# Optimization experiments

Measured on AMD Instinct MI355X. Metric: run time of the kernel, lower is better.

## Reference

```python
import jax, jax.numpy as jnp
import numpy as np

N_ATOMS = 65536
N_PAIRS = N_ATOMS * 32
MAXZ = 95          # D3 tables cover H..Pu, indexed directly by atomic number
NREF = 5           # number of reference coordination numbers per element
CUTOFF, CUTON = 12.0, 10.0   # model units; distances_model2Bohr == 1
K1, K3 = 16.0, -4.0
SMALL = 1e-30      # fp32 stand-in for the original's 1e-300 double guard


def setup_inputs() -> dict:
    key = jax.random.key(0)
    k0, k1, k2, k3 = jax.random.split(key, 4)
    rng = np.random.default_rng(0)

    atomic_numbers = jax.random.randint(k0, (N_ATOMS,), 1, 87)
    idx_i = jax.random.randint(k1, (N_PAIRS,), 0, N_ATOMS)
    idx_j = jax.random.randint(k2, (N_PAIRS,), 0, N_ATOMS)
    # pair distances spanning inside/switch/outside of the 10..12 cutoff band
    distances = jax.random.uniform(k3, (N_PAIRS,), minval=0.8, maxval=12.5)

    # synthetic stand-ins for the grimme_d3 data files
    rcov = jnp.asarray(rng.uniform(0.5, 3.0, (MAXZ,)).astype(np.float32))
    rcn_np = rng.uniform(0.0, 5.0, (MAXZ, NREF)).astype(np.float32)
    rcn_np[::3, NREF - 1] = -1.0  # mimic -1 padding for missing references
    rcn = jnp.asarray(rcn_np)
    rc6 = jnp.asarray(rng.uniform(1.0, 50.0, (MAXZ, MAXZ, NREF, NREF)).astype(np.float32))
    r2r4 = jnp.asarray(rng.uniform(1.0, 10.0, (MAXZ,)).astype(np.float32))

    s6 = jnp.float32(1.0)
    s8 = jnp.float32(0.9171)
    a1 = jnp.float32(0.3385)
    a2 = jnp.float32(2.883)
    return dict(distances=distances, rcov=rcov, rcn=rcn, rc6=rc6, r2r4=r2r4,
                s6=s6, s8=s8, a1=a1, a2=a2,
                atomic_numbers=atomic_numbers, idx_i=idx_i, idx_j=idx_j)


def reference(distances, rcov, rcn, rc6, r2r4, s6, s8, a1, a2,
              atomic_numbers, idx_i, idx_j):
    n = atomic_numbers.shape[0]
    zi = atomic_numbers[idx_i]
    zj = atomic_numbers[idx_j]

    # smooth switch-off from 1 (r < cuton) to 0 (r >= cutoff)
    x = (CUTOFF - distances) / (CUTOFF - CUTON)
    sw = jnp.where(distances < CUTON, 1.0,
                   jnp.where(distances >= CUTOFF, 0.0,
                             ((6.0 * x - 15.0) * x + 10.0) * x * x * x))

    # coordination numbers via inverse damping, scatter-summed per atom i
    rcov_ij = rcov[zi] + rcov[zj]
    cn_ij = sw / (1.0 + jnp.exp(-K1 * (rcov_ij / distances - 1.0)))
    cn = jax.ops.segment_sum(cn_ij, idx_i, num_segments=n)  # [N]

    # Gaussian weights over reference CNs (soft retrieval into rc6 table)
    rcn_a = rcn[atomic_numbers]                 # [N, NREF]
    mask = rcn_a >= 0
    dcn = rcn_a - cn[:, None]
    gw = jnp.where(mask, jnp.exp(K3 * dcn * dcn), 0.0)
    norm = jnp.sum(gw, axis=-1, keepdims=True)
    # exceptional case: all gaussians underflow -> pick the max reference CN
    rcn_max_a = jnp.max(rcn, axis=-1)[atomic_numbers][:, None]
    exceptional = (rcn_a == rcn_max_a).astype(gw.dtype)
    weights = jnp.where(norm == 0, exceptional, gw / jnp.maximum(norm, SMALL))  # [N, NREF]

    # weighted pairwise C6 from reference table rc6[Zi, Zj, a, b]
    w_i = weights[idx_i]                         # [P, NREF]
    w_j = weights[idx_j]                         # [P, NREF]
    c6 = jnp.einsum('pa,pb,pab->p', w_i, w_j, rc6[zi, zj])

    # C8 = 3 * C6 * <r2>/<r4>_i * <r2>/<r4>_j ; BJ critical radius
    qq = 3.0 * r2r4[zi] * r2r4[zj]
    rr = a1 * jnp.sqrt(qq) + a2

    d2 = distances * distances
    d6 = d2 * d2 * d2
    d8 = d6 * d2
    rr2 = rr * rr
    rr6 = rr2 * rr2 * rr2
    rr8 = rr6 * rr2

    # BJ-damped dispersion energy per pair (0.5 for double counting), switched
    e_pair = -0.5 * (s6 * c6 / (d6 + rr6) + s8 * qq * c6 / (d8 + rr8)) * sw

    # per-atom dispersion energies (energies_Hartree2model == 1)
    return jax.ops.segment_sum(e_pair, idx_i, num_segments=n)
```

## Files before the change

kernel.cpp:

```cpp
#include <hip/hip_runtime.h>
#include <stdint.h>


typedef unsigned short u16;
#define MAXZ 95
#define NREF 5
#define EXC_CUT -87.33654f
#define NB    1024
#define BSH   6
#define BSZ   64
#define CAPSH 12
#define SBLOCKS 128
#define RC_TOTAL (MAXZ * MAXZ * 32)

__device__ __forceinline__ float h2f(u16 h) {
    union { _Float16 h; u16 u; } v; v.u = h; return (float)v.h;
}
__device__ __forceinline__ u16 f2h(float f) {
    union { _Float16 h; u16 u; } v; v.h = (_Float16)f; return v.u;
}

__device__ __forceinline__ float switch_fn(float d) {
    if (d < 10.0f) return 1.0f;
    float x = (12.0f - d) * 0.5f;
    return ((6.0f * x - 15.0f) * x + 10.0f) * x * x * x;
}

__device__ __forceinline__ void calc_weights(const float* __restrict__ rcn_z,
                                             float cni, float* __restrict__ w) {
    float r[NREF], arg[NREF];
    float rmax = -1e30f, marg = -1e30f;
#pragma unroll
    for (int a = 0; a < NREF; a++) {
        r[a] = rcn_z[a];
        rmax = fmaxf(rmax, r[a]);
        float dc = r[a] - cni;
        arg[a] = (-4.0f * dc) * dc;
        if (r[a] >= 0.0f) marg = fmaxf(marg, arg[a]);
    }
    if (marg < EXC_CUT) {
#pragma unroll
        for (int a = 0; a < NREF; a++) w[a] = (r[a] == rmax) ? 1.0f : 0.0f;
    } else {
        float g[NREF], norm = 0.0f;
#pragma unroll
        for (int a = 0; a < NREF; a++) {
            float e = (r[a] >= 0.0f) ? expf(arg[a]) : 0.0f;
            g[a] = e;
            norm += e;
        }
        float inv = 1.0f / fmaxf(norm, 1e-30f);
#pragma unroll
        for (int a = 0; a < NREF; a++) w[a] = g[a] * inv;
    }
}

__global__ __launch_bounds__(1024) void scatter_pairs(const float* __restrict__ dist,
                                                      const int* __restrict__ idx_i,
                                                      const int* __restrict__ idx_j,
                                                      const int* __restrict__ Z,
                                                      const float* __restrict__ rcov,
                                                      const float* __restrict__ rc6,
                                                      float* __restrict__ rcovA,
                                                      u16* __restrict__ rc6pad,
                                                      uint32_t* __restrict__ bcount,
                                                      uint2* __restrict__ recs,
                                                      int n_pairs, int n_atoms,
                                                      int chunk) {
    __shared__ uint32_t hist[NB];
    __shared__ uint32_t run[NB];

    int g = blockIdx.x * 1024 + (int)threadIdx.x;
    int T = gridDim.x * 1024;
    for (int i = g; i < n_atoms; i += T) rcovA[i] = rcov[Z[i]];
    for (int id = g; id < RC_TOTAL; id += T) {
        int tile = id >> 5, slot = id & 31;
        rc6pad[id] = (slot < 25) ? f2h(rc6[(size_t)tile * 25 + slot]) : (u16)0;
    }

    for (int t = threadIdx.x; t < NB; t += 1024) hist[t] = 0;
    __syncthreads();
    int lo = blockIdx.x * chunk;
    int hi = min(lo + chunk, n_pairs);

    for (int q0 = lo + (int)threadIdx.x * 4; q0 < hi; q0 += 4096) {
        int m = min(4, hi - q0);
        float d4[4];
        int i4[4];
        if (m == 4) {
            float4 dv = *(const float4*)(dist + q0);
            int4 iv = *(const int4*)(idx_i + q0);
            d4[0] = dv.x; d4[1] = dv.y; d4[2] = dv.z; d4[3] = dv.w;
            i4[0] = iv.x; i4[1] = iv.y; i4[2] = iv.z; i4[3] = iv.w;
        } else {
            for (int s = 0; s < m; s++) { d4[s] = dist[q0 + s]; i4[s] = idx_i[q0 + s]; }
        }
#pragma unroll
        for (int s = 0; s < 4; s++) {
            if (s < m && d4[s] < 12.0f)
                atomicAdd(&hist[((uint32_t)i4[s]) >> BSH], 1u);
        }
    }
    __syncthreads();
    for (int t = threadIdx.x; t < NB; t += 1024) {
        uint32_t h = hist[t];
        run[t] = h ? atomicAdd(&bcount[t], h) : 0u;
    }
    __syncthreads();

    for (int q0 = lo + (int)threadIdx.x * 4; q0 < hi; q0 += 4096) {
        int m = min(4, hi - q0);
        float d4[4];
        int i4[4], j4[4];
        if (m == 4) {
            float4 dv = *(const float4*)(dist + q0);
            int4 iv = *(const int4*)(idx_i + q0);
            int4 jv = *(const int4*)(idx_j + q0);
            d4[0] = dv.x; d4[1] = dv.y; d4[2] = dv.z; d4[3] = dv.w;
            i4[0] = iv.x; i4[1] = iv.y; i4[2] = iv.z; i4[3] = iv.w;
            j4[0] = jv.x; j4[1] = jv.y; j4[2] = jv.z; j4[3] = jv.w;
        } else {
            for (int s = 0; s < m; s++) {
                d4[s] = dist[q0 + s]; i4[s] = idx_i[q0 + s]; j4[s] = idx_j[q0 + s];
            }
        }
#pragma unroll
        for (int s = 0; s < 4; s++) {
            if (s >= m) continue;
            float d = d4[s];
            if (d >= 12.0f) continue;
            uint32_t i = (uint32_t)i4[s];
            uint32_t b = i >> BSH;
            uint32_t pos = atomicAdd(&run[b], 1u);
            if (pos < (1u << CAPSH)) {
                uint32_t packed = ((uint32_t)j4[s] & 0xFFFFu) |
                                  ((i & (BSZ - 1u)) << 16);
                recs[((size_t)b << CAPSH) + pos] = make_uint2(__float_as_uint(d), packed);
            }
        }
    }
}

__global__ __launch_bounds__(256) void cn_weights_bucket(const uint2* __restrict__ recs,
                                                         const uint32_t* __restrict__ bcount,
                                                         const float* __restrict__ rcovA,
                                                         const int* __restrict__ Z,
                                                         const float* __restrict__ rcn,
                                                         const float* __restrict__ r2r4,
                                                         uint4* __restrict__ arec_h,
                                                         int n_atoms) {
    __shared__ float lrc[BSZ];
    __shared__ float acc[BSZ];
    int b = blockIdx.x;
    int base = b << BSH;
    if (threadIdx.x < BSZ) {
        int i = base + (int)threadIdx.x;
        lrc[threadIdx.x] = (i < n_atoms) ? rcovA[i] : 0.0f;
        acc[threadIdx.x] = 0.0f;
    }
    __syncthreads();
    uint32_t n = min(bcount[b], 1u << CAPSH);
    const uint2* r0 = recs + ((size_t)b << CAPSH);
    for (uint32_t k = threadIdx.x; k < n; k += 256) {
        uint2 r = r0[k];
        float d = __uint_as_float(r.x);
        int j  = r.y & 0xFFFF;
        int il = r.y >> 16;
        float rij = lrc[il] + rcovA[j];
        float sw = switch_fn(d);
        atomicAdd(&acc[il], sw / (1.0f + expf(-16.0f * (rij / d - 1.0f))));
    }
    __syncthreads();
    if (threadIdx.x < BSZ) {
        int i = base + (int)threadIdx.x;
        if (i < n_atoms) {
            int z = Z[i];
            float w[NREF];
            calc_weights(rcn + (size_t)z * NREF, acc[threadIdx.x], w);
            uint4 pk;
            pk.x = (uint32_t)f2h(w[0]) | ((uint32_t)f2h(w[1]) << 16);
            pk.y = (uint32_t)f2h(w[2]) | ((uint32_t)f2h(w[3]) << 16);
            pk.z = (uint32_t)f2h(w[4]) | ((uint32_t)f2h(r2r4[z]) << 16);
            pk.w = (uint32_t)z;
            arec_h[i] = pk;
        }
    }
}

__global__ __launch_bounds__(256) void energy_bucket(const uint2* __restrict__ recs,
                                                     const uint32_t* __restrict__ bcount,
                                                     const uint4* __restrict__ arec_h,
                                                     const u16* __restrict__ rc6pad,
                                                     const float* __restrict__ s6p,
                                                     const float* __restrict__ s8p,
                                                     const float* __restrict__ a1p,
                                                     const float* __restrict__ a2p,
                                                     float* __restrict__ eout,
                                                     int n_atoms) {
    __shared__ float4 la0[BSZ];
    __shared__ float4 la1[BSZ];
    __shared__ float  acc[BSZ];
    int b = blockIdx.x;
    int base = b << BSH;
    if (threadIdx.x < BSZ) {
        int i = min(base + (int)threadIdx.x, n_atoms - 1);
        uint4 pk = arec_h[i];
        la0[threadIdx.x] = make_float4(h2f(pk.x & 0xFFFFu), h2f(pk.x >> 16),
                                       h2f(pk.y & 0xFFFFu), h2f(pk.y >> 16));
        la1[threadIdx.x] = make_float4(h2f(pk.z & 0xFFFFu), h2f(pk.z >> 16),
                                       __int_as_float((int)pk.w), 0.0f);
        acc[threadIdx.x] = 0.0f;
    }
    __syncthreads();
    float s6 = s6p[0], s8 = s8p[0], a1 = a1p[0], a2 = a2p[0];
    uint32_t n = min(bcount[b], 1u << CAPSH);
    const uint2* r0 = recs + ((size_t)b << CAPSH);
    for (uint32_t k = threadIdx.x; k < n; k += 256) {
        uint2 r = r0[k];
        float d = __uint_as_float(r.x);
        int j  = r.y & 0xFFFF;
        int il = r.y >> 16;
        float4 ai0 = la0[il];
        float4 ai1 = la1[il];
        uint4 pj = arec_h[j];
        float wj[NREF] = {h2f(pj.x & 0xFFFFu), h2f(pj.x >> 16),
                          h2f(pj.y & 0xFFFFu), h2f(pj.y >> 16),
                          h2f(pj.z & 0xFFFFu)};
        float r2r4j = h2f(pj.z >> 16);
        int zi = __float_as_int(ai1.z);
        int zj = (int)pj.w;
        float wi[NREF] = {ai0.x, ai0.y, ai0.z, ai0.w, ai1.x};

        const uint4* T4 = (const uint4*)(rc6pad + (size_t)(zi * MAXZ + zj) * 32);
        uint4 t0 = T4[0], t1 = T4[1], t2 = T4[2];
        uint32_t t3 = ((const uint32_t*)T4)[12];
        float tt[25];
        uint32_t tw[12] = {t0.x, t0.y, t0.z, t0.w, t1.x, t1.y, t1.z, t1.w,
                           t2.x, t2.y, t2.z, t2.w};
#pragma unroll
        for (int k2 = 0; k2 < 12; k2++) {
            tt[2 * k2]     = h2f((u16)(tw[k2] & 0xFFFFu));
            tt[2 * k2 + 1] = h2f((u16)(tw[k2] >> 16));
        }
        tt[24] = h2f((u16)(t3 & 0xFFFFu));

        float c6 = 0.0f;
#pragma unroll
        for (int a = 0; a < NREF; a++) {
            float ss = 0.0f;
#pragma unroll
            for (int bb = 0; bb < NREF; bb++) ss = fmaf(wj[bb], tt[a * NREF + bb], ss);
            c6 = fmaf(wi[a], ss, c6);
        }

        float qq = 3.0f * ai1.y * r2r4j;
        float rr = a1 * sqrtf(qq) + a2;
        float d2 = d * d;
        float d6 = d2 * d2 * d2;
        float d8 = d6 * d2;
        float rr2 = rr * rr;
        float rr6 = rr2 * rr2 * rr2;
        float rr8 = rr6 * rr2;
        float sw = switch_fn(d);

        float e = -0.5f * (s6 * c6 / (d6 + rr6) + s8 * qq * c6 / (d8 + rr8)) * sw;
        atomicAdd(&acc[il], e);
    }
    __syncthreads();
    if (threadIdx.x < BSZ) {
        int i = base + (int)threadIdx.x;
        if (i < n_atoms) eout[i] = acc[threadIdx.x];
    }
}

__global__ __launch_bounds__(256) void pair_cn_slim(const float* __restrict__ dist,
                                                    const float* __restrict__ rcov,
                                                    const int* __restrict__ Z,
                                                    const int* __restrict__ idx_i,
                                                    const int* __restrict__ idx_j,
                                                    float* __restrict__ cn,
                                                    int n_pairs) {
    int p = blockIdx.x * blockDim.x + threadIdx.x;
    if (p >= n_pairs) return;
    float d = dist[p];
    if (d >= 12.0f) return;
    float rij = rcov[Z[idx_i[p]]] + rcov[Z[idx_j[p]]];
    float sw = switch_fn(d);
    atomicAdd(&cn[idx_i[p]], sw / (1.0f + expf(-16.0f * (rij / d - 1.0f))));
}

__global__ __launch_bounds__(256) void pair_energy_slim(const float* __restrict__ dist,
                                                        const int* __restrict__ Z,
                                                        const int* __restrict__ idx_i,
                                                        const int* __restrict__ idx_j,
                                                        const float* __restrict__ cn,
                                                        const float* __restrict__ rcn,
                                                        const float* __restrict__ r2r4,
                                                        const float* __restrict__ rc6,
                                                        const float* __restrict__ s6p,
                                                        const float* __restrict__ s8p,
                                                        const float* __restrict__ a1p,
                                                        const float* __restrict__ a2p,
                                                        float* __restrict__ eout,
                                                        int n_pairs) {
    int p = blockIdx.x * blockDim.x + threadIdx.x;
    if (p >= n_pairs) return;
    float d = dist[p];
    if (d >= 12.0f) return;
    int i = idx_i[p], j = idx_j[p];
    int zi = Z[i], zj = Z[j];
    float wi[NREF], wj[NREF];
    calc_weights(rcn + (size_t)zi * NREF, cn[i], wi);
    calc_weights(rcn + (size_t)zj * NREF, cn[j], wj);
    const float* T = rc6 + (size_t)(zi * MAXZ + zj) * 25;
    float c6 = 0.0f;
#pragma unroll
    for (int a = 0; a < NREF; a++) {
        float s = 0.0f;
#pragma unroll
        for (int bb = 0; bb < NREF; bb++) s = fmaf(wj[bb], T[a * NREF + bb], s);
        c6 = fmaf(wi[a], s, c6);
    }
    float qq = 3.0f * r2r4[zi] * r2r4[zj];
    float rr = a1p[0] * sqrtf(qq) + a2p[0];
    float d2 = d * d;
    float d6 = d2 * d2 * d2;
    float d8 = d6 * d2;
    float rr2 = rr * rr;
    float rr6 = rr2 * rr2 * rr2;
    float rr8 = rr6 * rr2;
    float sw = switch_fn(d);
    float e = -0.5f * (s6p[0] * c6 / (d6 + rr6) + s8p[0] * qq * c6 / (d8 + rr8)) * sw;
    atomicAdd(&eout[i], e);
}

extern "C" void kernel_launch(void* const* d_in, const int* in_sizes, int n_in,
                              void* d_out, int out_size, void* d_ws, size_t ws_size,
                              hipStream_t stream) {
    const float* dist = (const float*)d_in[0];
    const float* rcov = (const float*)d_in[1];
    const float* rcn  = (const float*)d_in[2];
    const float* rc6  = (const float*)d_in[3];
    const float* r2r4 = (const float*)d_in[4];
    const float* s6p  = (const float*)d_in[5];
    const float* s8p  = (const float*)d_in[6];
    const float* a1p  = (const float*)d_in[7];
    const float* a2p  = (const float*)d_in[8];
    const int* Z    = (const int*)d_in[9];
    const int* idxi = (const int*)d_in[10];
    const int* idxj = (const int*)d_in[11];
    float* out = (float*)d_out;

    int n_pairs = in_sizes[0];
    int n_atoms = in_sizes[9];

    char* ws = (char*)d_ws;
    size_t o_bcount = 0;
    size_t o_rcovA  = 4096;
    size_t o_arec   = (o_rcovA + (size_t)n_atoms * 4 + 15) & ~(size_t)15;
    size_t o_rc6    = (o_arec + (size_t)n_atoms * 16 + 63) & ~(size_t)63;
    size_t o_recs   = (o_rc6 + (size_t)RC_TOTAL * 2 + 255) & ~(size_t)255;
    size_t need     = o_recs + ((size_t)NB << CAPSH) * 8;

    uint32_t* bcount = (uint32_t*)(ws + o_bcount);
    float* rcovA  = (float*)(ws + o_rcovA);
    uint4* arec_h = (uint4*)(ws + o_arec);
    u16*   rcpad  = (u16*)(ws + o_rc6);
    uint2* recs   = (uint2*)(ws + o_recs);

    if (ws_size >= need && n_atoms <= NB * BSZ && n_atoms <= 65536) {
        hipMemsetAsync(bcount, 0, NB * 4, stream);
        int chunk = (n_pairs + SBLOCKS - 1) / SBLOCKS;
        scatter_pairs<<<SBLOCKS, 1024, 0, stream>>>(dist, idxi, idxj, Z, rcov, rc6,
                                                    rcovA, rcpad, bcount, recs,
                                                    n_pairs, n_atoms, chunk);
        cn_weights_bucket<<<NB, 256, 0, stream>>>(recs, bcount, rcovA, Z, rcn, r2r4,
                                                  arec_h, n_atoms);
        energy_bucket<<<NB, 256, 0, stream>>>(recs, bcount, arec_h, rcpad,
                                              s6p, s8p, a1p, a2p, out, n_atoms);
    } else {
        int pgrid = (n_pairs + 255) / 256;
        float* cn = (float*)(ws + o_rcovA);
        hipMemsetAsync(out, 0, (size_t)n_atoms * 4, stream);
        hipMemsetAsync(cn, 0, (size_t)n_atoms * 4, stream);
        pair_cn_slim<<<pgrid, 256, 0, stream>>>(dist, rcov, Z, idxi, idxj, cn, n_pairs);
        pair_energy_slim<<<pgrid, 256, 0, stream>>>(dist, Z, idxi, idxj, cn, rcn, r2r4,
                                                    rc6, s6p, s8p, a1p, a2p, out, n_pairs);
    }
}
```

Before: 147.2 us.

## Pack neighbor atomic number into pair records to remove gathers

The scatter kernel now gathers Z[j] once per in-cutoff pair and packs it into the upper bits of the record word. The CN kernel then looks up rcov from a shared-memory table indexed by that Z instead of gathering a per-atom rcovA array, which is no longer built. The energy kernel takes zj from the record so the rc6 tile load can be issued before the arec_h[j] gather, and the loads are reordered to overlap. This adds a random Z gather in the scatter pass and relies on j fitting in 16 bits and Z in 7 bits.

```diff
diff --git a/kernel.cpp b/kernel.cpp
--- a/kernel.cpp
+++ b/kernel.cpp
@@ -59,20 +59,16 @@
                                                       const int* __restrict__ idx_i,
                                                       const int* __restrict__ idx_j,
                                                       const int* __restrict__ Z,
-                                                      const float* __restrict__ rcov,
                                                       const float* __restrict__ rc6,
-                                                      float* __restrict__ rcovA,
                                                       u16* __restrict__ rc6pad,
                                                       uint32_t* __restrict__ bcount,
                                                       uint2* __restrict__ recs,
-                                                      int n_pairs, int n_atoms,
-                                                      int chunk) {
+                                                      int n_pairs, int chunk) {
     __shared__ uint32_t hist[NB];
     __shared__ uint32_t run[NB];
 
     int g = blockIdx.x * 1024 + (int)threadIdx.x;
     int T = gridDim.x * 1024;
-    for (int i = g; i < n_atoms; i += T) rcovA[i] = rcov[Z[i]];
     for (int id = g; id < RC_TOTAL; id += T) {
         int tile = id >> 5, slot = id & 31;
         rc6pad[id] = (slot < 25) ? f2h(rc6[(size_t)tile * 25 + slot]) : (u16)0;
@@ -111,7 +107,7 @@
     for (int q0 = lo + (int)threadIdx.x * 4; q0 < hi; q0 += 4096) {
         int m = min(4, hi - q0);
         float d4[4];
-        int i4[4], j4[4];
+        int i4[4], j4[4], zj4[4];
         if (m == 4) {
             float4 dv = *(const float4*)(dist + q0);
             int4 iv = *(const int4*)(idx_i + q0);
@@ -125,6 +121,9 @@
             }
         }
 #pragma unroll
+        for (int s = 0; s < 4; s++)
+            if (s < m && d4[s] < 12.0f) zj4[s] = Z[j4[s]];
+#pragma unroll
         for (int s = 0; s < 4; s++) {
             if (s >= m) continue;
             float d = d4[s];
@@ -134,7 +133,8 @@
             uint32_t pos = atomicAdd(&run[b], 1u);
             if (pos < (1u << CAPSH)) {
                 uint32_t packed = ((uint32_t)j4[s] & 0xFFFFu) |
-                                  ((i & (BSZ - 1u)) << 16);
+                                  ((i & (BSZ - 1u)) << 16) |
+                                  ((uint32_t)zj4[s] << 22);
                 recs[((size_t)b << CAPSH) + pos] = make_uint2(__float_as_uint(d), packed);
             }
         }
@@ -143,19 +143,24 @@
 
 __global__ __launch_bounds__(256) void cn_weights_bucket(const uint2* __restrict__ recs,
                                                          const uint32_t* __restrict__ bcount,
-                                                         const float* __restrict__ rcovA,
+                                                         const float* __restrict__ rcov,
                                                          const int* __restrict__ Z,
                                                          const float* __restrict__ rcn,
                                                          const float* __restrict__ r2r4,
                                                          uint4* __restrict__ arec_h,
                                                          int n_atoms) {
+    __shared__ float lrcov[MAXZ + 1];
     __shared__ float lrc[BSZ];
     __shared__ float acc[BSZ];
     int b = blockIdx.x;
     int base = b << BSH;
+    if (threadIdx.x <= MAXZ) {
+        int t = threadIdx.x;
+        lrcov[t] = (t < MAXZ) ? rcov[t] : 0.0f;
+    }
     if (threadIdx.x < BSZ) {
         int i = base + (int)threadIdx.x;
-        lrc[threadIdx.x] = (i < n_atoms) ? rcovA[i] : 0.0f;
+        lrc[threadIdx.x] = (i < n_atoms) ? rcov[Z[i]] : 0.0f;
         acc[threadIdx.x] = 0.0f;
     }
     __syncthreads();
@@ -164,9 +169,9 @@
     for (uint32_t k = threadIdx.x; k < n; k += 256) {
         uint2 r = r0[k];
         float d = __uint_as_float(r.x);
-        int j  = r.y & 0xFFFF;
-        int il = r.y >> 16;
-        float rij = lrc[il] + rcovA[j];
+        int il = (r.y >> 16) & 0x3F;
+        int zj = (r.y >> 22) & 0x7F;
+        float rij = lrc[il] + lrcov[zj];
         float sw = switch_fn(d);
         atomicAdd(&acc[il], sw / (1.0f + expf(-16.0f * (rij / d - 1.0f))));
     }
@@ -219,21 +224,23 @@
         uint2 r = r0[k];
         float d = __uint_as_float(r.x);
         int j  = r.y & 0xFFFF;
-        int il = r.y >> 16;
+        int il = (r.y >> 16) & 0x3F;
+        int zj = (r.y >> 22) & 0x7F;
+        float4 ai1 = la1[il];
+        int zi = __float_as_int(ai1.z);
+
+        const uint4* T4 = (const uint4*)(rc6pad + (size_t)(zi * MAXZ + zj) * 32);
+        uint4 t0 = T4[0], t1 = T4[1], t2 = T4[2];
+        uint32_t t3 = ((const uint32_t*)T4)[12];
+        uint4 pj = arec_h[j];
+
         float4 ai0 = la0[il];
-        float4 ai1 = la1[il];
-        uint4 pj = arec_h[j];
+        float wi[NREF] = {ai0.x, ai0.y, ai0.z, ai0.w, ai1.x};
         float wj[NREF] = {h2f(pj.x & 0xFFFFu), h2f(pj.x >> 16),
                           h2f(pj.y & 0xFFFFu), h2f(pj.y >> 16),
                           h2f(pj.z & 0xFFFFu)};
         float r2r4j = h2f(pj.z >> 16);
-        int zi = __float_as_int(ai1.z);
-        int zj = (int)pj.w;
-        float wi[NREF] = {ai0.x, ai0.y, ai0.z, ai0.w, ai1.x};
-
-        const uint4* T4 = (const uint4*)(rc6pad + (size_t)(zi * MAXZ + zj) * 32);
-        uint4 t0 = T4[0], t1 = T4[1], t2 = T4[2];
-        uint32_t t3 = ((const uint32_t*)T4)[12];
+
         float tt[25];
         uint32_t tw[12] = {t0.x, t0.y, t0.z, t0.w, t1.x, t1.y, t1.z, t1.w,
                            t2.x, t2.y, t2.z, t2.w};
@@ -356,14 +363,12 @@
 
     char* ws = (char*)d_ws;
     size_t o_bcount = 0;
-    size_t o_rcovA  = 4096;
-    size_t o_arec   = (o_rcovA + (size_t)n_atoms * 4 + 15) & ~(size_t)15;
+    size_t o_arec   = 4096;
     size_t o_rc6    = (o_arec + (size_t)n_atoms * 16 + 63) & ~(size_t)63;
     size_t o_recs   = (o_rc6 + (size_t)RC_TOTAL * 2 + 255) & ~(size_t)255;
     size_t need     = o_recs + ((size_t)NB << CAPSH) * 8;
 
     uint32_t* bcount = (uint32_t*)(ws + o_bcount);
-    float* rcovA  = (float*)(ws + o_rcovA);
     uint4* arec_h = (uint4*)(ws + o_arec);
     u16*   rcpad  = (u16*)(ws + o_rc6);
     uint2* recs   = (uint2*)(ws + o_recs);
@@ -371,16 +376,16 @@
     if (ws_size >= need && n_atoms <= NB * BSZ && n_atoms <= 65536) {
         hipMemsetAsync(bcount, 0, NB * 4, stream);
         int chunk = (n_pairs + SBLOCKS - 1) / SBLOCKS;
-        scatter_pairs<<<SBLOCKS, 1024, 0, stream>>>(dist, idxi, idxj, Z, rcov, rc6,
-                                                    rcovA, rcpad, bcount, recs,
-                                                    n_pairs, n_atoms, chunk);
-        cn_weights_bucket<<<NB, 256, 0, stream>>>(recs, bcount, rcovA, Z, rcn, r2r4,
+        scatter_pairs<<<SBLOCKS, 1024, 0, stream>>>(dist, idxi, idxj, Z, rc6,
+                                                    rcpad, bcount, recs,
+                                                    n_pairs, chunk);
+        cn_weights_bucket<<<NB, 256, 0, stream>>>(recs, bcount, rcov, Z, rcn, r2r4,
                                                   arec_h, n_atoms);
         energy_bucket<<<NB, 256, 0, stream>>>(recs, bcount, arec_h, rcpad,
                                               s6p, s8p, a1p, a2p, out, n_atoms);
     } else {
         int pgrid = (n_pairs + 255) / 256;
-        float* cn = (float*)(ws + o_rcovA);
+        float* cn = (float*)(ws + o_arec);
         hipMemsetAsync(out, 0, (size_t)n_atoms * 4, stream);
         hipMemsetAsync(cn, 0, (size_t)n_atoms * 4, stream);
         pair_cn_slim<<<pgrid, 256, 0, stream>>>(dist, rcov, Z, idxi, idxj, cn, n_pairs);
```

Measured after the change: 157.0 us. +6.6%, slower.
